# Optimization experiments

Hardware: AMD Instinct MI355X
Metric: run time of the kernel (lower is better)

Reference implementation:

```python
import jax, jax.numpy as jnp
import numpy as np
from jax import lax

B, N, M = 4, 16384, 512
RADIUS2 = 4.0        # radius=2 (hard-coded in forward), compare squared distances
BALL_K = 64          # k=64 hard-coded in forward
KNN_K = 9            # opt.node_knn_k_1
SIGMA_LB = 0.001     # opt.loss_sigma_lower_bound

_DIMS = [("conv1", 6, 64), ("conv2", 64, 64), ("conv3", 64, 64),
         ("conv4", 128, 128), ("conv5", 128, 128),
         ("knnb1", 131, 256), ("knnb2", 256, 256), ("knnb3", 256, 256),
         ("knna1", 512, 512), ("knna2", 512, 512),
         ("mlp1", 640, 512), ("mlp2", 512, 256)]


def setup_inputs() -> dict:
    key = jax.random.key(0)
    ks = jax.random.split(key, 6)
    inp = {
        "x": jax.random.normal(ks[0], (B, 3, N), jnp.float32),
        "sn": jax.random.normal(ks[1], (B, 3, N), jnp.float32),
        "node": jax.random.normal(ks[2], (B, 3, M), jnp.float32),
    }
    for i, (name, cin, cout) in enumerate(_DIMS):
        k = jax.random.fold_in(ks[3], i)
        inp[name + "_w"] = jax.random.normal(k, (cout, cin), jnp.float32) * np.float32(1.0 / np.sqrt(cin))
        inp[name + "_b"] = jnp.zeros((cout,), jnp.float32)
    inp["mlp3_w"] = jax.random.normal(ks[4], (4, 256), jnp.float32) * np.float32(1e-4)  # .normal_(0, 0.0001)
    inp["mlp3_b"] = jnp.zeros((4,), jnp.float32)
    return inp


def _conv(f, w, b, act=True):
    # 1x1 conv over (B,C,M) or (B,C,M,K): channel matmul + bias (+relu)
    y = jnp.einsum('oc,bc...->bo...', w, f) + b.reshape((1, -1) + (1,) * (f.ndim - 2))
    return jax.nn.relu(y) if act else y


def _sqdist(a, b):
    # a: (B,3,Ma), b: (B,3,Nb) -> (B,Ma,Nb) squared euclidean distances
    aa = jnp.sum(a * a, axis=1)
    bb = jnp.sum(b * b, axis=1)
    ab = jnp.einsum('bcm,bcn->bmn', a, b)
    return aa[:, :, None] + bb[:, None, :] - 2.0 * ab


def _gather(feat, idx):
    # feat: (B,C,Nb), idx: (B,Mq,K) -> (B,C,Mq,K)
    Bq, C, _ = feat.shape
    _, Mq, K = idx.shape
    flat = jnp.broadcast_to(idx.reshape(Bq, 1, Mq * K), (Bq, C, Mq * K))
    return jnp.take_along_axis(feat, flat, axis=2).reshape(Bq, C, Mq, K)


def _ball_query(sqd, radius2, k):
    # first k point indices (in original order) with dist<radius, padded by the first hit
    n = sqd.shape[2]
    mask = sqd < radius2
    keyi = jnp.where(mask, jnp.arange(n, dtype=jnp.int32)[None, None, :], jnp.int32(n))
    _, idx = lax.top_k(-keyi, k)  # k smallest keys == first k in-ball indices
    count = jnp.sum(mask, axis=2, keepdims=True)
    return jnp.where(jnp.arange(k)[None, None, :] < count, idx, idx[:, :, :1])


def reference(x, sn, node,
              conv1_w, conv1_b, conv2_w, conv2_b, conv3_w, conv3_b,
              conv4_w, conv4_b, conv5_w, conv5_b,
              knnb1_w, knnb1_b, knnb2_w, knnb2_b, knnb3_w, knnb3_b,
              knna1_w, knna1_b, knna2_w, knna2_b,
              mlp1_w, mlp1_b, mlp2_w, mlp2_b, mlp3_w, mlp3_b):
    x_aug = jnp.concatenate([x, sn], axis=1)                      # (B,6,N)
    idx = _ball_query(_sqdist(node, x), RADIUS2, BALL_K)          # (B,M,64)
    xb = _gather(x_aug, idx)                                      # (B,6,M,64)
    xb = jnp.concatenate([xb[:, :3] - node[:, :, :, None], xb[:, 3:]], axis=1)
    f = _conv(_conv(_conv(xb, conv1_w, conv1_b), conv2_w, conv2_b), conv3_w, conv3_b)
    fmax = jnp.max(f, axis=3, keepdims=True)
    f = jnp.concatenate([f, jnp.broadcast_to(fmax, f.shape)], axis=1)
    f = _conv(_conv(f, conv4_w, conv4_b), conv5_w, conv5_b)
    feat1 = jnp.max(f, axis=3)                                    # (B,128,M)

    # GeneralKNNFusionModule: query=node, database=node, x=feat1, K=KNN_K
    _, knn_idx = lax.top_k(-_sqdist(node, node), KNN_K)           # (B,M,K) nearest nodes
    coords = _gather(node, knn_idx) - node[:, :, :, None]         # (B,3,M,K)
    g = jnp.concatenate([coords, _gather(feat1, knn_idx)], axis=1)  # (B,131,M,K)
    g = _conv(_conv(_conv(g, knnb1_w, knnb1_b), knnb2_w, knnb2_b), knnb3_w, knnb3_b)
    gmax = jnp.max(g, axis=3, keepdims=True)
    g = jnp.concatenate([g, jnp.broadcast_to(gmax, g.shape)], axis=1)
    g = _conv(_conv(g, knna1_w, knna1_b), knna2_w, knna2_b)
    feat2 = jnp.max(g, axis=3)                                    # (B,512,M)

    h = jnp.concatenate([feat1, feat2], axis=1)                   # (B,640,M)
    h = _conv(_conv(h, mlp1_w, mlp1_b), mlp2_w, mlp2_b)
    ksig = _conv(h, mlp3_w, mlp3_b, act=False)                    # (B,4,M)
    keypoints = ksig[:, :3] + node
    sigmas = jax.nn.softplus(ksig[:, 3]) + SIGMA_LB
    return node, keypoints, sigmas
```

## Files before the change

### kernel.cpp

```cpp
#include <hip/hip_runtime.h>

typedef unsigned short u16;
typedef unsigned int u32;
typedef __bf16 bf16x8 __attribute__((ext_vector_type(8)));
typedef float floatx4 __attribute__((ext_vector_type(4)));
typedef unsigned short u16x8 __attribute__((ext_vector_type(8)));
typedef unsigned int u32x4 __attribute__((ext_vector_type(4)));

static constexpr int B_ = 4;
static constexpr int N_ = 16384;
static constexpr int M_ = 512;

__device__ __forceinline__ u16 f2bf(float f) {
    u32 u = __float_as_uint(f);
    u32 r = (u + 0x7fffu + ((u >> 16) & 1u)) >> 16;
    return (u16)r;
}
__device__ __forceinline__ float bf2f(u16 x) {
    return __uint_as_float(((u32)x) << 16);
}
__device__ __forceinline__ u32 pack2(float a, float b) {
    return (u32)f2bf(a) | ((u32)f2bf(b) << 16);
}

struct WConvArgs { const float* src[12]; };

__global__ __launch_bounds__(256) void prep_kernel(
    const float* __restrict__ x, const float* __restrict__ node,
    int* __restrict__ idx, int* __restrict__ knn,
    WConvArgs wa, u16* __restrict__ Wbf) {
    int bid = blockIdx.x;
    int tid = threadIdx.x, wave = tid >> 6, lane = tid & 63;

    if (bid < 2048) {
        int bm = bid;
        int b = bm >> 9, m = bm & 511;
        __shared__ int sidx[4][64];
        __shared__ int scnt[4];
        const float* xb = x + (size_t)b * 3 * N_;
        float nx = node[((size_t)b * 3 + 0) * M_ + m];
        float ny = node[((size_t)b * 3 + 1) * M_ + m];
        float nz = node[((size_t)b * 3 + 2) * M_ + m];
        float aa = nx * nx + ny * ny + nz * nz;
        int cnt = 0;
        int base = wave * 4096;
        for (int n0 = base; n0 < base + 4096; n0 += 256) {
            float px[4], py[4], pz[4];
#pragma unroll
            for (int i = 0; i < 4; ++i) {
                int n = n0 + i * 64 + lane;
                px[i] = xb[n]; py[i] = xb[N_ + n]; pz[i] = xb[2 * N_ + n];
            }
#pragma unroll
            for (int i = 0; i < 4; ++i) {
                float bb = px[i] * px[i] + py[i] * py[i] + pz[i] * pz[i];
                float d = aa + bb - 2.0f * (nx * px[i] + ny * py[i] + nz * pz[i]);
                bool inb = d < 4.0f;
                unsigned long long mask = __ballot(inb);
                if (inb && cnt < 64) {
                    int pos = cnt + __popcll(mask & ((1ull << lane) - 1ull));
                    if (pos < 64) sidx[wave][pos] = n0 + i * 64 + lane;
                }
                cnt += __popcll(mask);
            }
            if (cnt >= 64) break;
        }
        if (lane == 0) scnt[wave] = cnt;
        __syncthreads();
        if (tid < 64) {
            int total = scnt[0] + scnt[1] + scnt[2] + scnt[3];
            int v = 0;
            if (total > 0) {
                int lim = total < 64 ? total : 64;
                int slot = tid < lim ? tid : 0;
                int w = 0, pre = 0;
                while (w < 3 && slot >= pre + scnt[w]) { pre += scnt[w]; ++w; }
                v = sidx[w][slot - pre];
            }
            idx[(size_t)bm * 64 + tid] = v;
        }
    } else if (bid < 2560) {
        int bm = (bid - 2048) * 4 + wave;
        int b = bm >> 9, m = bm & 511;
        const float* nb = node + (size_t)b * 3 * M_;
        float nx = nb[m], ny = nb[M_ + m], nz = nb[2 * M_ + m];
        float aa = nx * nx + ny * ny + nz * nz;
        float dist[8];
        int didx[8];
#pragma unroll
        for (int i = 0; i < 8; ++i) {
            int n = lane + i * 64;
            float px = nb[n], py = nb[M_ + n], pz = nb[2 * M_ + n];
            float bb = px * px + py * py + pz * pz;
            float ab = nx * px + ny * py + nz * pz;
            dist[i] = aa + bb - 2.0f * ab;
            didx[i] = n;
        }
        for (int r = 0; r < 9; ++r) {
            float bv = dist[0]; int bi = didx[0]; int bslot = 0;
#pragma unroll
            for (int i = 1; i < 8; ++i) {
                if (dist[i] < bv || (dist[i] == bv && didx[i] < bi)) {
                    bv = dist[i]; bi = didx[i]; bslot = i;
                }
            }
            float rv = bv; int ri = bi;
            for (int off = 32; off > 0; off >>= 1) {
                float ov = __shfl_down(rv, off);
                int   oi = __shfl_down(ri, off);
                if (ov < rv || (ov == rv && oi < ri)) { rv = ov; ri = oi; }
            }
            ri = __shfl(ri, 0);
            if (lane == 0) knn[(size_t)bm * 9 + r] = ri;
            if (bi == ri) dist[bslot] = 3.0e38f;
        }
    } else {
        const int CI[12] = {6, 64, 64, 128, 128, 131, 256, 256, 512, 512, 640, 512};
        const int KP[12] = {32, 64, 64, 128, 128, 160, 256, 256, 512, 512, 640, 512};
        const int OFF[13] = {0, 2048, 6144, 10240, 26624, 43008, 83968, 149504,
                             215040, 477184, 739328, 1067008, 1198080};
        int e = (bid - 2560) * 256 + tid;
        int w = 0;
        while (e >= OFF[w + 1]) ++w;
        int local = e - OFF[w];
        int kp = KP[w];
        int co = local / kp, k = local - co * kp;
        float v = 0.0f;
        if (w == 5) {
            if (k < 3) v = wa.src[5][(size_t)co * 131 + k];
            else if (k >= 8 && k < 136) v = wa.src[5][(size_t)co * 131 + (k - 5)];
        } else if (k < CI[w]) {
            v = wa.src[w][(size_t)co * CI[w] + k];
        }
        Wbf[e] = f2bf(v);
    }
}

static constexpr int RS = 136;

__device__ __forceinline__ bf16x8 ldsA(const u16* act, int rf, int l15, int quad, int ks) {
    return *(const bf16x8*)(act + (rf * 16 + l15) * RS + ks * 32 + quad * 8);
}
__device__ __forceinline__ bf16x8 ldW(const u16* W, int ks, int l15, int quad, int kstride) {
    return *(const bf16x8*)(W + (size_t)l15 * kstride + ks * 32 + quad * 8);
}

__global__ __launch_bounds__(256, 2) void fused_stage1_kernel(
    const float* __restrict__ x, const float* __restrict__ sn,
    const float* __restrict__ node, const int* __restrict__ idx,
    const u16* __restrict__ Wbf,
    const float* __restrict__ b1, const float* __restrict__ b2,
    const float* __restrict__ b3, const float* __restrict__ b4,
    const float* __restrict__ b5, u16* __restrict__ h) {
    __shared__ __align__(16) u16 act[256 * RS];
    __shared__ __align__(16) u16 mv[4][64];
    int blk = blockIdx.x;
    int bm0 = blk * 4;
    int tid = threadIdx.x, wave = tid >> 6, lane = tid & 63;
    int quad = lane >> 4, l15 = lane & 15;

    {
        int row = tid;
        int bm = bm0 + (row >> 6);
        int b = bm >> 9, m = bm & 511;
        int j = idx[(size_t)bm * 64 + (row & 63)];
        const float* xb = x + (size_t)b * 3 * N_;
        const float* sb = sn + (size_t)b * 3 * N_;
        float c0 = xb[j]          - node[((size_t)b * 3 + 0) * M_ + m];
        float c1 = xb[N_ + j]     - node[((size_t)b * 3 + 1) * M_ + m];
        float c2 = xb[2 * N_ + j] - node[((size_t)b * 3 + 2) * M_ + m];
        float s0 = sb[j], s1 = sb[N_ + j], s2 = sb[2 * N_ + j];
        u16* r = act + row * RS;
        *(u32*)(r)     = pack2(c0, c1);
        *(u32*)(r + 2) = pack2(c2, s0);
        *(u32*)(r + 4) = pack2(s1, s2);
        *(u32*)(r + 6) = 0u;
        u32x4* z = (u32x4*)(r + 8);
        z[0] = (u32x4){0u, 0u, 0u, 0u};
        z[1] = (u32x4){0u, 0u, 0u, 0u};
        z[2] = (u32x4){0u, 0u, 0u, 0u};
    }
    __syncthreads();

    {
        const u16* Wp = Wbf + (size_t)(wave * 16) * 32;
        bf16x8 bw = ldW(Wp, 0, l15, quad, 32);
        floatx4 c[16];
#pragma unroll
        for (int rf = 0; rf < 16; ++rf) {
            bf16x8 a = ldsA(act, rf, l15, quad, 0);
            c[rf] = __builtin_amdgcn_mfma_f32_16x16x32_bf16(a, bw, (floatx4){0.f,0.f,0.f,0.f}, 0, 0, 0);
        }
        float bias = b1[wave * 16 + l15];
        __syncthreads();
#pragma unroll
        for (int rf = 0; rf < 16; ++rf)
#pragma unroll
            for (int r = 0; r < 4; ++r)
                act[(rf * 16 + quad * 4 + r) * RS + wave * 16 + l15] = f2bf(fmaxf(c[rf][r] + bias, 0.0f));
        __syncthreads();
    }

    const int WOFF23[2] = {2048, 6144};
    const float* bp23[2] = {b2, b3};
#pragma unroll 1
    for (int cv = 0; cv < 2; ++cv) {
        const u16* Wp = Wbf + WOFF23[cv] + (size_t)(wave * 16) * 64;
        bf16x8 bw0 = ldW(Wp, 0, l15, quad, 64);
        bf16x8 bw1 = ldW(Wp, 1, l15, quad, 64);
        floatx4 c[16] = {};
#pragma unroll
        for (int ks = 0; ks < 2; ++ks)
#pragma unroll
            for (int rf = 0; rf < 16; ++rf) {
                bf16x8 a = ldsA(act, rf, l15, quad, ks);
                c[rf] = __builtin_amdgcn_mfma_f32_16x16x32_bf16(a, ks ? bw1 : bw0, c[rf], 0, 0, 0);
            }
        float bias = bp23[cv][wave * 16 + l15];
        float mxN[4] = {0.0f, 0.0f, 0.0f, 0.0f};
#pragma unroll
        for (int rf = 0; rf < 16; ++rf)
#pragma unroll
            for (int r = 0; r < 4; ++r) {
                float v = fmaxf(c[rf][r] + bias, 0.0f);
                mxN[rf >> 2] = fmaxf(mxN[rf >> 2], v);
            }
        __syncthreads();
#pragma unroll
        for (int rf = 0; rf < 16; ++rf)
#pragma unroll
            for (int r = 0; r < 4; ++r)
                act[(rf * 16 + quad * 4 + r) * RS + wave * 16 + l15] = f2bf(fmaxf(c[rf][r] + bias, 0.0f));
        if (cv == 1) {
#pragma unroll
            for (int n = 0; n < 4; ++n) {
                float mx = mxN[n];
                mx = fmaxf(mx, __shfl_xor(mx, 16));
                mx = fmaxf(mx, __shfl_xor(mx, 32));
                if (quad == 0) mv[n][wave * 16 + l15] = f2bf(mx);
            }
        }
        __syncthreads();
    }

    {
        const u16* Wp = Wbf + 10240 + (size_t)(wave * 32) * 128;
        bf16x8 bw[2][4];
#pragma unroll
        for (int cf = 0; cf < 2; ++cf)
#pragma unroll
            for (int ks = 0; ks < 4; ++ks)
                bw[cf][ks] = ldW(Wp + (size_t)cf * 16 * 128, ks, l15, quad, 128);
        floatx4 c[16][2] = {};
#pragma unroll
        for (int ks = 0; ks < 4; ++ks)
#pragma unroll
            for (int rf = 0; rf < 16; ++rf) {
                bf16x8 a = (ks < 2) ? ldsA(act, rf, l15, quad, ks)
                                    : *(const bf16x8*)(&mv[rf >> 2][(ks - 2) * 32 + quad * 8]);
#pragma unroll
                for (int cf = 0; cf < 2; ++cf)
                    c[rf][cf] = __builtin_amdgcn_mfma_f32_16x16x32_bf16(a, bw[cf][ks], c[rf][cf], 0, 0, 0);
            }
        float bias[2];
#pragma unroll
        for (int cf = 0; cf < 2; ++cf) bias[cf] = b4[wave * 32 + cf * 16 + l15];
        __syncthreads();
#pragma unroll
        for (int rf = 0; rf < 16; ++rf)
#pragma unroll
            for (int cf = 0; cf < 2; ++cf)
#pragma unroll
                for (int r = 0; r < 4; ++r)
                    act[(rf * 16 + quad * 4 + r) * RS + wave * 32 + cf * 16 + l15] =
                        f2bf(fmaxf(c[rf][cf][r] + bias[cf], 0.0f));
        __syncthreads();
    }

    {
        const u16* Wp = Wbf + 26624 + (size_t)(wave * 32) * 128;
        bf16x8 bw[2][4];
#pragma unroll
        for (int cf = 0; cf < 2; ++cf)
#pragma unroll
            for (int ks = 0; ks < 4; ++ks)
                bw[cf][ks] = ldW(Wp + (size_t)cf * 16 * 128, ks, l15, quad, 128);
        floatx4 c[16][2] = {};
#pragma unroll
        for (int ks = 0; ks < 4; ++ks)
#pragma unroll
            for (int rf = 0; rf < 16; ++rf) {
                bf16x8 a = ldsA(act, rf, l15, quad, ks);
#pragma unroll
                for (int cf = 0; cf < 2; ++cf)
                    c[rf][cf] = __builtin_amdgcn_mfma_f32_16x16x32_bf16(a, bw[cf][ks], c[rf][cf], 0, 0, 0);
            }
#pragma unroll
        for (int cf = 0; cf < 2; ++cf) {
            float bias = b5[wave * 32 + cf * 16 + l15];
            float mxN[4] = {0.0f, 0.0f, 0.0f, 0.0f};
#pragma unroll
            for (int rf = 0; rf < 16; ++rf)
#pragma unroll
                for (int r = 0; r < 4; ++r) {
                    float v = fmaxf(c[rf][cf][r] + bias, 0.0f);
                    mxN[rf >> 2] = fmaxf(mxN[rf >> 2], v);
                }
#pragma unroll
            for (int n = 0; n < 4; ++n) {
                float mx = mxN[n];
                mx = fmaxf(mx, __shfl_xor(mx, 16));
                mx = fmaxf(mx, __shfl_xor(mx, 32));
                if (quad == 0)
                    h[(size_t)(bm0 + n) * 640 + wave * 32 + cf * 16 + l15] = f2bf(mx);
            }
        }
    }
}

template <int KS, int CF, int RF, int PF, int RSx>
__device__ __forceinline__ void conv_inplace(u16* act, const u16* __restrict__ W0, int KP,
                                             const float* __restrict__ bias, int cb,
                                             int l15, int quad) {
    floatx4 acc[RF][CF];
#pragma unroll
    for (int rf = 0; rf < RF; ++rf)
#pragma unroll
        for (int cf = 0; cf < CF; ++cf) acc[rf][cf] = (floatx4){0.f, 0.f, 0.f, 0.f};

    bf16x8 bw[PF][CF];
#pragma unroll
    for (int p = 0; p < PF - 1; ++p)
        if (p < KS)
#pragma unroll
            for (int cf = 0; cf < CF; ++cf)
                bw[p][cf] = *(const bf16x8*)(W0 + (size_t)(cb + cf * 16 + l15) * KP +
                                             p * 32 + quad * 8);

#pragma unroll
    for (int ks = 0; ks < KS; ++ks) {
        if (ks + PF - 1 < KS) {
#pragma unroll
            for (int cf = 0; cf < CF; ++cf)
                bw[(ks + PF - 1) & (PF - 1)][cf] =
                    *(const bf16x8*)(W0 + (size_t)(cb + cf * 16 + l15) * KP +
                                     (ks + PF - 1) * 32 + quad * 8);
        }
#pragma unroll
        for (int rf = 0; rf < RF; ++rf) {
            bf16x8 a = *(const bf16x8*)(act + (rf * 16 + l15) * RSx + ks * 32 + quad * 8);
#pragma unroll
            for (int cf = 0; cf < CF; ++cf)
                acc[rf][cf] = __builtin_amdgcn_mfma_f32_16x16x32_bf16(a, bw[ks & (PF - 1)][cf], acc[rf][cf], 0, 0, 0);
        }
    }
    __syncthreads();
#pragma unroll
    for (int cf = 0; cf < CF; ++cf) {
        float bs = bias[cb + cf * 16 + l15];
#pragma unroll
        for (int rf = 0; rf < RF; ++rf)
#pragma unroll
            for (int r = 0; r < 4; ++r)
                act[(rf * 16 + quad * 4 + r) * RSx + cb + cf * 16 + l15] =
                    f2bf(fmaxf(acc[rf][cf][r] + bs, 0.0f));
    }
    __syncthreads();
}

static constexpr int RS2 = 520;

__global__ __launch_bounds__(256, 2) void fused_stage2_kernel(
    const float* __restrict__ node, u16* __restrict__ h, const int* __restrict__ knn,
    const u16* __restrict__ Wbf,
    const float* __restrict__ bb1, const float* __restrict__ bb2,
    const float* __restrict__ bb3, const float* __restrict__ ba1,
    const float* __restrict__ ba2) {
    __shared__ __align__(16) u16 act[48 * RS2];
    int blk = blockIdx.x;
    int node0 = blk * 4;
    int b = node0 >> 9;
    int tid = threadIdx.x, wave = tid >> 6, lane = tid & 63;
    int quad = lane >> 4, l15 = lane & 15;
    (void)lane;

    for (int e = tid; e < 48 * 20; e += 256)
        *(u16x8*)(act + (e / 20) * RS2 + (e % 20) * 8) = (u16x8){0,0,0,0,0,0,0,0};
    for (int e = tid; e < 12 * 44; e += 256)
        *(u16x8*)(act + (36 + e / 44) * RS2 + 160 + (e % 44) * 8) = (u16x8){0,0,0,0,0,0,0,0};
    __syncthreads();
    for (int e = tid; e < 36 * 3; e += 256) {
        int r = e / 3, c = e - r * 3;
        int nodei = node0 + r / 9;
        int j = knn[(size_t)nodei * 9 + (r % 9)];
        float v = node[((size_t)b * 3 + c) * M_ + j] - node[((size_t)b * 3 + c) * M_ + (nodei & 511)];
        act[r * RS2 + c] = f2bf(v);
    }
    for (int e = tid; e < 36 * 16; e += 256) {
        int r = e >> 4, s = e & 15;
        int nodei = node0 + r / 9;
        int j = knn[(size_t)nodei * 9 + (r % 9)];
        *(u16x8*)(act + r * RS2 + 8 + s * 8) =
            *(const u16x8*)(h + (size_t)(b * 512 + j) * 640 + s * 8);
    }
    __syncthreads();

    conv_inplace<5, 4, 3, 4, RS2>(act, Wbf + 43008, 160, bb1, wave * 64, l15, quad);
    conv_inplace<8, 4, 3, 4, RS2>(act, Wbf + 83968, 256, bb2, wave * 64, l15, quad);
    conv_inplace<8, 4, 3, 4, RS2>(act, Wbf + 149504, 256, bb3, wave * 64, l15, quad);

    for (int e = tid; e < 4 * 32; e += 256) {
        int li = e >> 5, s = e & 31;
        int r0 = li * 9;
        float mx[8];
#pragma unroll
        for (int i = 0; i < 8; ++i) mx[i] = -3.0e38f;
#pragma unroll
        for (int kk = 0; kk < 9; ++kk) {
            u16x8 v = *(const u16x8*)(act + (r0 + kk) * RS2 + s * 8);
#pragma unroll
            for (int i = 0; i < 8; ++i) mx[i] = fmaxf(mx[i], bf2f(v[i]));
        }
        u16x8 o;
#pragma unroll
        for (int i = 0; i < 8; ++i) o[i] = f2bf(mx[i]);
#pragma unroll
        for (int kk = 0; kk < 9; ++kk)
            *(u16x8*)(act + (r0 + kk) * RS2 + 256 + s * 8) = o;
    }
    __syncthreads();

    conv_inplace<16, 8, 3, 2, RS2>(act, Wbf + 215040, 512, ba1, wave * 128, l15, quad);
    conv_inplace<16, 8, 3, 2, RS2>(act, Wbf + 477184, 512, ba2, wave * 128, l15, quad);

    for (int e = tid; e < 4 * 64; e += 256) {
        int li = e >> 6, s = e & 63;
        int r0 = li * 9;
        float mx[8];
#pragma unroll
        for (int i = 0; i < 8; ++i) mx[i] = -3.0e38f;
#pragma unroll
        for (int kk = 0; kk < 9; ++kk) {
            u16x8 v = *(const u16x8*)(act + (r0 + kk) * RS2 + s * 8);
#pragma unroll
            for (int i = 0; i < 8; ++i) mx[i] = fmaxf(mx[i], bf2f(v[i]));
        }
        u16x8 o;
#pragma unroll
        for (int i = 0; i < 8; ++i) o[i] = f2bf(mx[i]);
        *(u16x8*)(h + (size_t)(node0 + li) * 640 + 128 + s * 8) = o;
    }
}

static constexpr int RS3 = 648;

__global__ __launch_bounds__(512, 2) void fused_stage3_kernel(
    const float* __restrict__ node, const u16* __restrict__ h,
    const u16* __restrict__ Wbf,
    const float* __restrict__ bm1, const float* __restrict__ bm2,
    const float* __restrict__ w3, const float* __restrict__ b3,
    float* __restrict__ out) {
    __shared__ __align__(16) u16 act[16 * RS3];
    int blk = blockIdx.x;
    int node0 = blk * 8;
    int tid = threadIdx.x, lane = tid & 63, wave = tid >> 6;
    int quad = lane >> 4, l15 = lane & 15;

    for (int e = tid; e < 16 * 80; e += 512) {
        int r = e / 80, seg = e - r * 80;
        u16x8 v = (r < 8) ? *(const u16x8*)(h + (size_t)(node0 + r) * 640 + seg * 8)
                          : (u16x8){0,0,0,0,0,0,0,0};
        *(u16x8*)(act + r * RS3 + seg * 8) = v;
    }
    __syncthreads();

    conv_inplace<20, 4, 1, 4, RS3>(act, Wbf + 739328, 640, bm1, wave * 64, l15, quad);
    conv_inplace<16, 2, 1, 4, RS3>(act, Wbf + 1067008, 512, bm2, wave * 32, l15, quad);

    if (tid < 32) {
        int li = tid >> 2, oc = tid & 3;
        const u16* row = act + li * RS3;
        const float* wrow = w3 + oc * 256;
        float a = 0.0f;
        for (int c = 0; c < 256; c += 4) {
            a += bf2f(row[c]) * wrow[c];
            a += bf2f(row[c + 1]) * wrow[c + 1];
            a += bf2f(row[c + 2]) * wrow[c + 2];
            a += bf2f(row[c + 3]) * wrow[c + 3];
        }
        a += b3[oc];
        int nodei = node0 + li;
        int b = nodei >> 9, m = nodei & 511;
        if (oc < 3) {
            float nv = node[((size_t)b * 3 + oc) * M_ + m];
            out[((size_t)b * 3 + oc) * M_ + m] = nv;
            out[6144 + ((size_t)b * 3 + oc) * M_ + m] = nv + a;
        } else {
            out[12288 + nodei] = fmaxf(a, 0.0f) + log1pf(expf(-fabsf(a))) + 0.001f;
        }
    }
}

extern "C" void kernel_launch(void* const* d_in, const int* in_sizes, int n_in,
                              void* d_out, int out_size, void* d_ws, size_t ws_size,
                              hipStream_t stream) {
    (void)in_sizes; (void)n_in; (void)out_size; (void)ws_size;
    const float* x = (const float*)d_in[0];
    const float* sn = (const float*)d_in[1];
    const float* node = (const float*)d_in[2];
    const float* W[13];
    const float* Bs[13];
    for (int i = 0; i < 13; ++i) {
        W[i] = (const float*)d_in[3 + 2 * i];
        Bs[i] = (const float*)d_in[4 + 2 * i];
    }
    float* out = (float*)d_out;

    char* ws = (char*)d_ws;
    int* idx = (int*)(ws + 0);
    int* knn = (int*)(ws + 524288);
    u16* Wbf = (u16*)(ws + 598016);
    u16* h   = (u16*)(ws + 2994176);

    WConvArgs wa;
    for (int w = 0; w < 12; ++w) wa.src[w] = W[w];

    prep_kernel<<<7240, 256, 0, stream>>>(x, node, idx, knn, wa, Wbf);

    fused_stage1_kernel<<<512, 256, 0, stream>>>(x, sn, node, idx, Wbf,
                                                 Bs[0], Bs[1], Bs[2], Bs[3], Bs[4], h);
    fused_stage2_kernel<<<512, 256, 0, stream>>>(node, h, knn, Wbf,
                                                 Bs[5], Bs[6], Bs[7], Bs[8], Bs[9]);
    fused_stage3_kernel<<<256, 512, 0, stream>>>(node, h, Wbf, Bs[10], Bs[11],
                                                 W[12], Bs[12], out);
}
```

Before: 257.7 us.

## Fuse stage2 and stage3 kernels, processing eight nodes per block

```diff
diff --git a/kernel.cpp b/kernel.cpp
--- a/kernel.cpp
+++ b/kernel.cpp
@@ -369,34 +369,37 @@
 }
 
 static constexpr int RS2 = 520;
-
-__global__ __launch_bounds__(256, 2) void fused_stage2_kernel(
+static constexpr int RS3 = 648;
+
+__global__ __launch_bounds__(512, 2) void fused_stage23_kernel(
     const float* __restrict__ node, u16* __restrict__ h, const int* __restrict__ knn,
     const u16* __restrict__ Wbf,
     const float* __restrict__ bb1, const float* __restrict__ bb2,
     const float* __restrict__ bb3, const float* __restrict__ ba1,
-    const float* __restrict__ ba2) {
-    __shared__ __align__(16) u16 act[48 * RS2];
+    const float* __restrict__ ba2,
+    const float* __restrict__ bm1, const float* __restrict__ bm2,
+    const float* __restrict__ w3, const float* __restrict__ b3,
+    float* __restrict__ out) {
+    __shared__ __align__(16) u16 act[80 * RS2 + 16 * RS3];
+    u16* mlpT = act + 80 * RS2;
     int blk = blockIdx.x;
-    int node0 = blk * 4;
+    int node0 = blk * 8;
     int b = node0 >> 9;
     int tid = threadIdx.x, wave = tid >> 6, lane = tid & 63;
     int quad = lane >> 4, l15 = lane & 15;
     (void)lane;
 
-    for (int e = tid; e < 48 * 20; e += 256)
+    for (int e = tid; e < 80 * 20; e += 512)
         *(u16x8*)(act + (e / 20) * RS2 + (e % 20) * 8) = (u16x8){0,0,0,0,0,0,0,0};
-    for (int e = tid; e < 12 * 44; e += 256)
-        *(u16x8*)(act + (36 + e / 44) * RS2 + 160 + (e % 44) * 8) = (u16x8){0,0,0,0,0,0,0,0};
-    __syncthreads();
-    for (int e = tid; e < 36 * 3; e += 256) {
+    __syncthreads();
+    for (int e = tid; e < 72 * 3; e += 512) {
         int r = e / 3, c = e - r * 3;
         int nodei = node0 + r / 9;
         int j = knn[(size_t)nodei * 9 + (r % 9)];
         float v = node[((size_t)b * 3 + c) * M_ + j] - node[((size_t)b * 3 + c) * M_ + (nodei & 511)];
         act[r * RS2 + c] = f2bf(v);
     }
-    for (int e = tid; e < 36 * 16; e += 256) {
+    for (int e = tid; e < 72 * 16; e += 512) {
         int r = e >> 4, s = e & 15;
         int nodei = node0 + r / 9;
         int j = knn[(size_t)nodei * 9 + (r % 9)];
@@ -405,11 +408,11 @@
     }
     __syncthreads();
 
-    conv_inplace<5, 4, 3, 4, RS2>(act, Wbf + 43008, 160, bb1, wave * 64, l15, quad);
-    conv_inplace<8, 4, 3, 4, RS2>(act, Wbf + 83968, 256, bb2, wave * 64, l15, quad);
-    conv_inplace<8, 4, 3, 4, RS2>(act, Wbf + 149504, 256, bb3, wave * 64, l15, quad);
-
-    for (int e = tid; e < 4 * 32; e += 256) {
+    conv_inplace<5, 2, 5, 4, RS2>(act, Wbf + 43008, 160, bb1, wave * 32, l15, quad);
+    conv_inplace<8, 2, 5, 4, RS2>(act, Wbf + 83968, 256, bb2, wave * 32, l15, quad);
+    conv_inplace<8, 2, 5, 4, RS2>(act, Wbf + 149504, 256, bb3, wave * 32, l15, quad);
+
+    for (int e = tid; e < 8 * 32; e += 512) {
         int li = e >> 5, s = e & 31;
         int r0 = li * 9;
         float mx[8];
@@ -430,10 +433,10 @@
     }
     __syncthreads();
 
-    conv_inplace<16, 8, 3, 2, RS2>(act, Wbf + 215040, 512, ba1, wave * 128, l15, quad);
-    conv_inplace<16, 8, 3, 2, RS2>(act, Wbf + 477184, 512, ba2, wave * 128, l15, quad);
-
-    for (int e = tid; e < 4 * 64; e += 256) {
+    conv_inplace<16, 4, 5, 4, RS2>(act, Wbf + 215040, 512, ba1, wave * 64, l15, quad);
+    conv_inplace<16, 4, 5, 4, RS2>(act, Wbf + 477184, 512, ba2, wave * 64, l15, quad);
+
+    for (int e = tid; e < 8 * 64; e += 512) {
         int li = e >> 6, s = e & 63;
         int r0 = li * 9;
         float mx[8];
@@ -448,38 +451,25 @@
         u16x8 o;
 #pragma unroll
         for (int i = 0; i < 8; ++i) o[i] = f2bf(mx[i]);
-        *(u16x8*)(h + (size_t)(node0 + li) * 640 + 128 + s * 8) = o;
-    }
-}
-
-static constexpr int RS3 = 648;
-
-__global__ __launch_bounds__(512, 2) void fused_stage3_kernel(
-    const float* __restrict__ node, const u16* __restrict__ h,
-    const u16* __restrict__ Wbf,
-    const float* __restrict__ bm1, const float* __restrict__ bm2,
-    const float* __restrict__ w3, const float* __restrict__ b3,
-    float* __restrict__ out) {
-    __shared__ __align__(16) u16 act[16 * RS3];
-    int blk = blockIdx.x;
-    int node0 = blk * 8;
-    int tid = threadIdx.x, lane = tid & 63, wave = tid >> 6;
-    int quad = lane >> 4, l15 = lane & 15;
-
-    for (int e = tid; e < 16 * 80; e += 512) {
+        *(u16x8*)(mlpT + li * RS3 + 128 + s * 8) = o;
+    }
+    for (int e = tid; e < 8 * 16; e += 512) {
+        int li = e >> 4, s = e & 15;
+        *(u16x8*)(mlpT + li * RS3 + s * 8) =
+            *(const u16x8*)(h + (size_t)(node0 + li) * 640 + s * 8);
+    }
+    for (int e = tid; e < 8 * 80; e += 512) {
         int r = e / 80, seg = e - r * 80;
-        u16x8 v = (r < 8) ? *(const u16x8*)(h + (size_t)(node0 + r) * 640 + seg * 8)
-                          : (u16x8){0,0,0,0,0,0,0,0};
-        *(u16x8*)(act + r * RS3 + seg * 8) = v;
-    }
-    __syncthreads();
-
-    conv_inplace<20, 4, 1, 4, RS3>(act, Wbf + 739328, 640, bm1, wave * 64, l15, quad);
-    conv_inplace<16, 2, 1, 4, RS3>(act, Wbf + 1067008, 512, bm2, wave * 32, l15, quad);
+        *(u16x8*)(mlpT + (8 + r) * RS3 + seg * 8) = (u16x8){0,0,0,0,0,0,0,0};
+    }
+    __syncthreads();
+
+    conv_inplace<20, 4, 1, 4, RS3>(mlpT, Wbf + 739328, 640, bm1, wave * 64, l15, quad);
+    conv_inplace<16, 2, 1, 4, RS3>(mlpT, Wbf + 1067008, 512, bm2, wave * 32, l15, quad);
 
     if (tid < 32) {
         int li = tid >> 2, oc = tid & 3;
-        const u16* row = act + li * RS3;
+        const u16* row = mlpT + li * RS3;
         const float* wrow = w3 + oc * 256;
         float a = 0.0f;
         for (int c = 0; c < 256; c += 4) {
@@ -490,11 +480,11 @@
         }
         a += b3[oc];
         int nodei = node0 + li;
-        int b = nodei >> 9, m = nodei & 511;
+        int bo = nodei >> 9, m = nodei & 511;
         if (oc < 3) {
-            float nv = node[((size_t)b * 3 + oc) * M_ + m];
-            out[((size_t)b * 3 + oc) * M_ + m] = nv;
-            out[6144 + ((size_t)b * 3 + oc) * M_ + m] = nv + a;
+            float nv = node[((size_t)bo * 3 + oc) * M_ + m];
+            out[((size_t)bo * 3 + oc) * M_ + m] = nv;
+            out[6144 + ((size_t)bo * 3 + oc) * M_ + m] = nv + a;
         } else {
             out[12288 + nodei] = fmaxf(a, 0.0f) + log1pf(expf(-fabsf(a))) + 0.001f;
         }
@@ -529,8 +519,7 @@
 
     fused_stage1_kernel<<<512, 256, 0, stream>>>(x, sn, node, idx, Wbf,
                                                  Bs[0], Bs[1], Bs[2], Bs[3], Bs[4], h);
-    fused_stage2_kernel<<<512, 256, 0, stream>>>(node, h, knn, Wbf,
-                                                 Bs[5], Bs[6], Bs[7], Bs[8], Bs[9]);
-    fused_stage3_kernel<<<256, 512, 0, stream>>>(node, h, Wbf, Bs[10], Bs[11],
-                                                 W[12], Bs[12], out);
-}
+    fused_stage23_kernel<<<256, 512, 0, stream>>>(node, h, knn, Wbf,
+                                                  Bs[5], Bs[6], Bs[7], Bs[8], Bs[9],
+                                                  Bs[10], Bs[11], W[12], Bs[12], out);
+}
```

Result: faster. 222.7 us (-13.6%).
